# Optimization experiments

Measured on AMD Instinct MI355X. Metric: run time of the kernel, lower is better.

## Reference

```python
import jax, jax.numpy as jnp
import numpy as np

HIDDEN = 256
B, SQ, SKV = 8, 2048, 2048
SCALE = float(np.sqrt(HIDDEN / 2.0))  # module uses sqrt(hidden_dim/2)


def setup_inputs() -> dict:
    key = jax.random.key(0)
    ks = jax.random.split(key, 9)
    s = 1.0 / np.sqrt(HIDDEN)
    return {
        "query": jax.random.normal(ks[0], (B, SQ, HIDDEN), jnp.float32),
        "key": jax.random.normal(ks[1], (B, SKV, HIDDEN), jnp.float32),
        "value": jax.random.normal(ks[2], (B, SKV, HIDDEN), jnp.float32),
        "Wq": jax.random.uniform(ks[3], (HIDDEN, HIDDEN), jnp.float32, -s, s),
        "bq": jax.random.uniform(ks[4], (HIDDEN,), jnp.float32, -s, s),
        "Wk": jax.random.uniform(ks[5], (HIDDEN, HIDDEN), jnp.float32, -s, s),
        "bk": jax.random.uniform(ks[6], (HIDDEN,), jnp.float32, -s, s),
        "Wv": jax.random.uniform(ks[7], (HIDDEN, HIDDEN), jnp.float32, -s, s),
        "bv": jax.random.uniform(ks[8], (HIDDEN,), jnp.float32, -s, s),
    }


def reference(query, key, value, Wq, bq, Wk, bk, Wv, bv):
    # Linear projections (torch Linear: x @ W.T + b)
    Q = jnp.einsum('bsd,ed->bse', query, Wq) + bq  # [B,SQ,H]
    K = jnp.einsum('bsd,ed->bse', key, Wk) + bk    # [B,SKV,H]
    V = jnp.einsum('bsd,ed->bse', value, Wv) + bv  # [B,SKV,H]
    scores = jnp.einsum('bqd,bkd->bqk', Q, K) / SCALE  # [B,SQ,SKV]
    weights = jax.nn.softmax(scores, axis=-1)
    return jnp.einsum('bqk,bkd->bqd', weights, V)  # [B,SQ,H]
```

## Files before the change

### kernel.cpp

```cpp
#include <hip/hip_runtime.h>

#define HID 256
#define NB 8
#define SQL 2048
#define SKV 2048
#define SPLIT 4
#define KPB (SKV / SPLIT)
#define KVB 64
#define NT (KPB / KVB)
#define NROW (NB * SQL)

typedef __attribute__((ext_vector_type(8))) short bf16x8;
typedef __attribute__((ext_vector_type(4))) float f32x4;
typedef __attribute__((ext_vector_type(16))) float f32x16;

static __device__ __forceinline__ unsigned short f2bf(float x) {
  union { float f; unsigned int u; } v; v.f = x;
  unsigned int r = v.u + 0x7FFFu + ((v.u >> 16) & 1u);
  return (unsigned short)(r >> 16);
}

__global__ void wconv_kernel(const float* __restrict__ Wq, const float* __restrict__ Wk,
                             const float* __restrict__ Wv, unsigned short* __restrict__ out) {
  int i = blockIdx.x * blockDim.x + threadIdx.x;
  if (i >= 3 * HID * HID) return;
  const float* src = (i < HID * HID) ? Wq : (i < 2 * HID * HID ? Wk : Wv);
  out[i] = f2bf(src[i & (HID * HID - 1)]);
}

__global__ __launch_bounds__(512, 4) void proj_kernel(
    const float* __restrict__ query, const float* __restrict__ key, const float* __restrict__ value,
    const unsigned short* __restrict__ Wb,
    const float* __restrict__ bq, const float* __restrict__ bk, const float* __restrict__ bv,
    unsigned short* __restrict__ Qb, unsigned short* __restrict__ Kb, unsigned short* __restrict__ Vtb) {
  __shared__ __align__(16) char wl[65536];
  int tid = threadIdx.x;
  int wave = tid >> 6, lane = tid & 63, lr = lane & 15, lg = lane >> 4;
  int blk = blockIdx.x;
  int mat = blk >> 8;
  int rem = blk & 255;
  int b = rem >> 5;
  int rt = (rem >> 1) & 15;
  int et = rem & 1;

  const float* X = (mat == 0) ? query : (mat == 1 ? key : value);
  const float* bias = (mat == 0) ? bq : (mat == 1 ? bk : bv);
  const char* Wsrc = (const char*)(Wb + mat * HID * HID + et * 128 * HID);

#pragma unroll
  for (int i = 0; i < 8; i++) {
    int c = i * 512 + tid;
    int e = c >> 5;
    int glo = e * 512 + (((c & 31) ^ (e & 7)) << 4);
    __builtin_amdgcn_global_load_lds(
        (const __attribute__((address_space(1))) unsigned int*)(Wsrc + glo),
        (__attribute__((address_space(3))) unsigned int*)(wl + c * 16), 16, 0, 0);
  }

  int row_a = rt * 128 + wave * 16 + lr;
  const float* xrow = X + ((size_t)(b * SQL + row_a)) * HID;
  bf16x8 af[8];
#pragma unroll
  for (int s = 0; s < 8; s++) {
    const float4* p = (const float4*)(xrow + s * 32 + lg * 8);
    float4 x0 = p[0], x1 = p[1];
    bf16x8 a;
    a[0] = (short)f2bf(x0.x); a[1] = (short)f2bf(x0.y); a[2] = (short)f2bf(x0.z); a[3] = (short)f2bf(x0.w);
    a[4] = (short)f2bf(x1.x); a[5] = (short)f2bf(x1.y); a[6] = (short)f2bf(x1.z); a[7] = (short)f2bf(x1.w);
    af[s] = a;
  }
  __syncthreads();

  int row_c = rt * 128 + wave * 16 + lg * 4;
#pragma unroll
  for (int eo = 0; eo < 8; eo++) {
    f32x4 acc = (f32x4){0.f, 0.f, 0.f, 0.f};
    int eL = eo * 16 + lr;
#pragma unroll
    for (int sl = 0; sl < 8; sl++) {
      bf16x8 bfr = *(const bf16x8*)(wl + eL * 512 + (((sl * 4 + lg) ^ (eL & 7)) << 4));
      acc = __builtin_amdgcn_mfma_f32_16x16x32_bf16(af[sl], bfr, acc, 0, 0, 0);
    }
    int e = et * 128 + eo * 16 + lr;
    float bv_ = bias[e];
    if (mat < 2) {
      unsigned short* dst = (mat == 0 ? Qb : Kb) + (size_t)(b * SQL) * HID;
#pragma unroll
      for (int i = 0; i < 4; i++)
        dst[(size_t)(row_c + i) * HID + e] = f2bf(acc[i] + bv_);
    } else {
      ushort4 v;
      v.x = f2bf(acc[0] + bv_); v.y = f2bf(acc[1] + bv_);
      v.z = f2bf(acc[2] + bv_); v.w = f2bf(acc[3] + bv_);
      *(ushort4*)(Vtb + ((size_t)(b * HID + e)) * SKV + row_c) = v;
    }
  }
}

__global__ __launch_bounds__(512, 2) void attn_kernel(
    const unsigned short* __restrict__ Qb, const unsigned short* __restrict__ Kb,
    const unsigned short* __restrict__ Vtb, unsigned short* __restrict__ Op,
    float* __restrict__ Ml) {
  extern __shared__ char smem[];
  int tid = threadIdx.x;
  int wave = tid >> 6, lane = tid & 63, l31 = lane & 31, h = lane >> 5;
  int L = (blockIdx.x & 7) * 32 + (blockIdx.x >> 3);
  int b = L >> 5, sp = (L >> 3) & 3, qt = L & 7;
  int q0 = qt * 256 + wave * 32;

  const char* Kc0 = (const char*)Kb + ((size_t)b * SKV + (size_t)sp * KPB) * (HID * 2);
  const char* Vc0 = (const char*)Vtb + (size_t)b * HID * SKV * 2 + (size_t)sp * KPB * 2;

  auto stage = [&](int t, char* kb, char* vb) {
    const char* Ks = Kc0 + t * (KVB * HID * 2);
    const char* Vs = Vc0 + t * (KVB * 2);
#pragma unroll
    for (int i = 0; i < 4; i++) {
      int g = i * 512 + tid;
      int ky = g >> 5, cs = g & 31;
      __builtin_amdgcn_global_load_lds(
          (const __attribute__((address_space(1))) unsigned int*)(Ks + ky * 512 + ((cs ^ (ky & 31)) << 4)),
          (__attribute__((address_space(3))) unsigned int*)(kb + g * 16), 16, 0, 0);
    }
#pragma unroll
    for (int i = 0; i < 4; i++) {
      int g = i * 512 + tid;
      int d = g >> 3, cs = g & 7;
      __builtin_amdgcn_global_load_lds(
          (const __attribute__((address_space(1))) unsigned int*)(Vs + (size_t)d * (SKV * 2) + ((cs ^ (d & 7)) << 4)),
          (__attribute__((address_space(3))) unsigned int*)(vb + g * 16), 16, 0, 0);
    }
  };

  bf16x8 qf[16];
  {
    const unsigned short* qrow = Qb + ((size_t)(b * SQL + q0 + l31)) * HID + h * 8;
#pragma unroll
    for (int s = 0; s < 16; s++) qf[s] = *(const bf16x8*)(qrow + s * 16);
  }

  f32x16 acc[8];
#pragma unroll
  for (int dt = 0; dt < 8; dt++)
#pragma unroll
    for (int j = 0; j < 16; j++) acc[dt][j] = 0.f;

  float m = -1e30f, lsum = 0.f;
  const float kC = 1.44269504088896341f / 11.3137084989847604f;

  auto substep = [&](const char* kb, const char* vb, int kt) {
    f32x16 p;
#pragma unroll
    for (int j = 0; j < 16; j++) p[j] = 0.f;
#pragma unroll
    for (int s = 0; s < 16; s++) {
      bf16x8 kf = *(const bf16x8*)(kb + (kt * 32 + l31) * 512 + (((2 * s + h) ^ l31) << 4));
      p = __builtin_amdgcn_mfma_f32_32x32x16_bf16(kf, qf[s], p, 0, 0, 0);
    }

    float tmax = p[0];
#pragma unroll
    for (int j = 1; j < 16; j++) tmax = fmaxf(tmax, p[j]);
    tmax = fmaxf(tmax, __shfl_xor(tmax, 32, 64));
    float msc = tmax * kC;
    if (!__all(msc <= m + 8.0f)) {
      float mn = fmaxf(m, msc);
      float al = exp2f(m - mn);
      lsum *= al;
      m = mn;
#pragma unroll
      for (int r = 0; r < 16; r++) {
        int qp = (r & 3) + 8 * (r >> 2) + 4 * h;
        float ar = __shfl(al, qp, 64);
#pragma unroll
        for (int dt = 0; dt < 8; dt++) acc[dt][r] *= ar;
      }
    }
#pragma unroll
    for (int j = 0; j < 16; j++) p[j] = exp2f(fmaf(p[j], kC, -m));
    float ts = 0.f;
#pragma unroll
    for (int j = 0; j < 16; j++) ts += p[j];
    ts += __shfl_xor(ts, 32, 64);
    lsum += ts;

#pragma unroll
    for (int k2 = 0; k2 < 2; k2++) {
      unsigned P0, P1, P2, P3;
      asm("v_cvt_pk_bf16_f32 %0, %1, %2" : "=v"(P0) : "v"(p[k2 * 8 + 0]), "v"(p[k2 * 8 + 1]));
      asm("v_cvt_pk_bf16_f32 %0, %1, %2" : "=v"(P1) : "v"(p[k2 * 8 + 2]), "v"(p[k2 * 8 + 3]));
      asm("v_cvt_pk_bf16_f32 %0, %1, %2" : "=v"(P2) : "v"(p[k2 * 8 + 4]), "v"(p[k2 * 8 + 5]));
      asm("v_cvt_pk_bf16_f32 %0, %1, %2" : "=v"(P3) : "v"(p[k2 * 8 + 6]), "v"(p[k2 * 8 + 7]));
      asm("v_permlane32_swap_b32 %0, %1" : "+v"(P0), "+v"(P2));
      asm("v_permlane32_swap_b32 %0, %1" : "+v"(P1), "+v"(P3));
      union { unsigned u[4]; bf16x8 v; } pa;
      pa.u[0] = P0; pa.u[1] = P1; pa.u[2] = P2; pa.u[3] = P3;
      int c = kt * 4 + k2 * 2 + h;
#pragma unroll
      for (int dt = 0; dt < 8; dt++) {
        bf16x8 vf = *(const bf16x8*)(vb + (dt * 32 + l31) * 128 + (((c ^ (l31 & 7)) & 7) << 4));
        acc[dt] = __builtin_amdgcn_mfma_f32_32x32x16_bf16(pa.v, vf, acc[dt], 0, 0, 0);
      }
    }
  };

  stage(0, smem, smem + 65536);
  for (int t = 0; t < NT; t++) {
    const char* kb = smem + (t & 1) * 32768;
    const char* vb = smem + 65536 + (t & 1) * 32768;
    if (t + 1 < NT) {
      stage(t + 1, smem + ((t + 1) & 1) * 32768, smem + 65536 + ((t + 1) & 1) * 32768);
      asm volatile("s_waitcnt vmcnt(8)" ::: "memory");
    } else {
      asm volatile("s_waitcnt vmcnt(0)" ::: "memory");
    }
    __builtin_amdgcn_s_barrier();
    __builtin_amdgcn_sched_barrier(0);
    substep(kb, vb, 0);
    substep(kb, vb, 1);
    __builtin_amdgcn_s_barrier();
  }

  if (h == 0) {
    float2 ml; ml.x = m; ml.y = lsum;
    *(float2*)(Ml + ((size_t)sp * NROW + (size_t)b * SQL + q0 + l31) * 2) = ml;
  }
#pragma unroll
  for (int r = 0; r < 16; r++) {
    int qp = (r & 3) + 8 * (r >> 2) + 4 * h;
    float linv = 1.0f / __shfl(lsum, qp, 64);
    size_t row = (size_t)b * SQL + q0 + qp;
#pragma unroll
    for (int dt = 0; dt < 8; dt++) {
      union { _Float16 hf; unsigned short u; } cv;
      cv.hf = (_Float16)(acc[dt][r] * linv);
      Op[((size_t)sp * NROW + row) * HID + dt * 32 + l31] = cv.u;
    }
  }
}

__global__ __launch_bounds__(256) void comb_kernel(const unsigned short* __restrict__ Op,
                                                   const float* __restrict__ Ml,
                                                   float* __restrict__ out) {
  int idx = blockIdx.x * 256 + threadIdx.x;
  int row = idx >> 6;
  int d0 = (idx & 63) << 2;
  float mv[SPLIT], lv[SPLIT];
#pragma unroll
  for (int s = 0; s < SPLIT; s++) {
    float2 ml = *(const float2*)(Ml + ((size_t)s * NROW + row) * 2);
    mv[s] = ml.x; lv[s] = ml.y;
  }
  float M = mv[0];
#pragma unroll
  for (int s = 1; s < SPLIT; s++) M = fmaxf(M, mv[s]);
  float W = 0.f, w[SPLIT];
#pragma unroll
  for (int s = 0; s < SPLIT; s++) { w[s] = lv[s] * exp2f(mv[s] - M); W += w[s]; }
  float wi = 1.0f / W;
  float o0 = 0.f, o1 = 0.f, o2 = 0.f, o3 = 0.f;
#pragma unroll
  for (int s = 0; s < SPLIT; s++) {
    ushort4 u = *(const ushort4*)(Op + ((size_t)s * NROW + row) * HID + d0);
    union { unsigned short us; _Float16 hf; } c0, c1, c2, c3;
    c0.us = u.x; c1.us = u.y; c2.us = u.z; c3.us = u.w;
    o0 += w[s] * (float)c0.hf; o1 += w[s] * (float)c1.hf;
    o2 += w[s] * (float)c2.hf; o3 += w[s] * (float)c3.hf;
  }
  float4 res; res.x = o0 * wi; res.y = o1 * wi; res.z = o2 * wi; res.w = o3 * wi;
  *(float4*)(out + (size_t)row * HID + d0) = res;
}

extern "C" void kernel_launch(void* const* d_in, const int* in_sizes, int n_in,
                              void* d_out, int out_size, void* d_ws, size_t ws_size,
                              hipStream_t stream) {
  const float* query = (const float*)d_in[0];
  const float* key   = (const float*)d_in[1];
  const float* value = (const float*)d_in[2];
  const float* Wq = (const float*)d_in[3];
  const float* bq = (const float*)d_in[4];
  const float* Wk = (const float*)d_in[5];
  const float* bk = (const float*)d_in[6];
  const float* Wv = (const float*)d_in[7];
  const float* bv = (const float*)d_in[8];

  char* ws = (char*)d_ws;
  unsigned short* Wb  = (unsigned short*)ws;
  unsigned short* Qb  = (unsigned short*)(ws + 393216);
  unsigned short* Kb  = Qb + (size_t)NB * SQL * HID;
  unsigned short* Vtb = Kb + (size_t)NB * SKV * HID;
  unsigned short* Op  = Vtb + (size_t)NB * HID * SKV;
  float* Ml = (float*)(Op + (size_t)SPLIT * NROW * HID);

  hipLaunchKernelGGL(wconv_kernel, dim3(768), dim3(256), 0, stream, Wq, Wk, Wv, Wb);
  hipLaunchKernelGGL(proj_kernel, dim3(768), dim3(512), 0, stream,
                     query, key, value, Wb, bq, bk, bv, Qb, Kb, Vtb);
  hipLaunchKernelGGL(attn_kernel, dim3(256), dim3(512), 131072, stream, Qb, Kb, Vtb, Op, Ml);
  hipLaunchKernelGGL(comb_kernel, dim3(4096), dim3(256), 0, stream, Op, Ml, (float*)d_out);
}
```

Baseline: 103.1 us.

## Software-pipeline QK of the next tile with PV of the previous tile

Attention blocks shrink to 4 waves covering 128 query rows, and the KV tile shrinks to 32 keys. The main loop is reordered so the QK MFMAs for tile t are issued next to the PV MFMAs for tile t-1. K uses double buffering and V uses triple buffering, and each iteration needs a single barrier instead of two. Global-to-LDS staging offsets are precomputed per thread, and the V LDS swizzle is changed. The goal is to hide softmax latency and barrier stalls behind matrix work, at the cost of more live registers (the bf16 P fragments are carried across iterations) and twice as many loop iterations.

```diff
diff --git a/kernel.cpp b/kernel.cpp
--- a/kernel.cpp
+++ b/kernel.cpp
@@ -6,7 +6,7 @@
 #define SKV 2048
 #define SPLIT 4
 #define KPB (SKV / SPLIT)
-#define KVB 64
+#define KVB 32
 #define NT (KPB / KVB)
 #define NROW (NB * SQL)
 
@@ -97,39 +97,47 @@
   }
 }
 
-__global__ __launch_bounds__(512, 2) void attn_kernel(
+__global__ __launch_bounds__(256, 2) void attn_kernel(
     const unsigned short* __restrict__ Qb, const unsigned short* __restrict__ Kb,
     const unsigned short* __restrict__ Vtb, unsigned short* __restrict__ Op,
     float* __restrict__ Ml) {
   extern __shared__ char smem[];
   int tid = threadIdx.x;
   int wave = tid >> 6, lane = tid & 63, l31 = lane & 31, h = lane >> 5;
-  int L = (blockIdx.x & 7) * 32 + (blockIdx.x >> 3);
-  int b = L >> 5, sp = (L >> 3) & 3, qt = L & 7;
-  int q0 = qt * 256 + wave * 32;
-
-  const char* Kc0 = (const char*)Kb + ((size_t)b * SKV + (size_t)sp * KPB) * (HID * 2);
-  const char* Vc0 = (const char*)Vtb + (size_t)b * HID * SKV * 2 + (size_t)sp * KPB * 2;
+  int L = (blockIdx.x & 7) * 64 + (blockIdx.x >> 3);
+  int b = L >> 6, sp = (L >> 4) & 3, qt = L & 15;
+  int q0 = qt * 128 + wave * 32;
+
+  const char* Kc0 = (const char*)(Kb + ((size_t)b * SKV + (size_t)sp * KPB) * HID);
+  const char* Vc0 = (const char*)(Vtb + (size_t)b * HID * SKV + (size_t)sp * KPB);
+
+  int offK[4], offV[4];
+#pragma unroll
+  for (int i = 0; i < 4; i++) {
+    int idx = i * 256 + tid;
+    int ky = idx >> 5, cs = idx & 31;
+    offK[i] = ky * 512 + ((cs ^ ky) << 4);
+    int rv = idx >> 3, pp = idx & 7;
+    int p = pp ^ (rv & 7);
+    int d = 2 * rv + (p >> 2), c = p & 3;
+    offV[i] = d * (SKV * 2) + c * 16;
+  }
 
   auto stage = [&](int t, char* kb, char* vb) {
     const char* Ks = Kc0 + t * (KVB * HID * 2);
     const char* Vs = Vc0 + t * (KVB * 2);
 #pragma unroll
-    for (int i = 0; i < 4; i++) {
-      int g = i * 512 + tid;
-      int ky = g >> 5, cs = g & 31;
+    for (int i = 0; i < 4; i++)
       __builtin_amdgcn_global_load_lds(
-          (const __attribute__((address_space(1))) unsigned int*)(Ks + ky * 512 + ((cs ^ (ky & 31)) << 4)),
-          (__attribute__((address_space(3))) unsigned int*)(kb + g * 16), 16, 0, 0);
-    }
-#pragma unroll
-    for (int i = 0; i < 4; i++) {
-      int g = i * 512 + tid;
-      int d = g >> 3, cs = g & 7;
+          (const __attribute__((address_space(1))) unsigned int*)(Ks + offK[i]),
+          (__attribute__((address_space(3))) unsigned int*)(kb + (i * 256 + tid) * 16),
+          16, 0, 0);
+#pragma unroll
+    for (int i = 0; i < 4; i++)
       __builtin_amdgcn_global_load_lds(
-          (const __attribute__((address_space(1))) unsigned int*)(Vs + (size_t)d * (SKV * 2) + ((cs ^ (d & 7)) << 4)),
-          (__attribute__((address_space(3))) unsigned int*)(vb + g * 16), 16, 0, 0);
-    }
+          (const __attribute__((address_space(1))) unsigned int*)(Vs + offV[i]),
+          (__attribute__((address_space(3))) unsigned int*)(vb + (i * 256 + tid) * 16),
+          16, 0, 0);
   };
 
   bf16x8 qf[16];
@@ -147,17 +155,35 @@
 
   float m = -1e30f, lsum = 0.f;
   const float kC = 1.44269504088896341f / 11.3137084989847604f;
-
-  auto substep = [&](const char* kb, const char* vb, int kt) {
+  bf16x8 pa0, pa1;
+
+  auto qk = [&](const char* kb) {
     f32x16 p;
 #pragma unroll
     for (int j = 0; j < 16; j++) p[j] = 0.f;
 #pragma unroll
     for (int s = 0; s < 16; s++) {
-      bf16x8 kf = *(const bf16x8*)(kb + (kt * 32 + l31) * 512 + (((2 * s + h) ^ l31) << 4));
+      bf16x8 kf = *(const bf16x8*)(kb + l31 * 512 + (((2 * s + h) ^ l31) << 4));
       p = __builtin_amdgcn_mfma_f32_32x32x16_bf16(kf, qf[s], p, 0, 0, 0);
     }
-
+    return p;
+  };
+
+  auto pv = [&](const char* vb) {
+#pragma unroll
+    for (int k2 = 0; k2 < 2; k2++) {
+      bf16x8 pav = (k2 == 0) ? pa0 : pa1;
+#pragma unroll
+      for (int dt = 0; dt < 8; dt++) {
+        int d = dt * 32 + l31;
+        int slot = (((d & 1) * 4 + k2 * 2 + h) ^ ((d >> 1) & 7));
+        bf16x8 vf = *(const bf16x8*)(vb + (d >> 1) * 128 + (slot << 4));
+        acc[dt] = __builtin_amdgcn_mfma_f32_32x32x16_bf16(pav, vf, acc[dt], 0, 0, 0);
+      }
+    }
+  };
+
+  auto sm = [&](f32x16 p) {
     float tmax = p[0];
 #pragma unroll
     for (int j = 1; j < 16; j++) tmax = fmaxf(tmax, p[j]);
@@ -184,42 +210,48 @@
     ts += __shfl_xor(ts, 32, 64);
     lsum += ts;
 
-#pragma unroll
-    for (int k2 = 0; k2 < 2; k2++) {
-      unsigned P0, P1, P2, P3;
-      asm("v_cvt_pk_bf16_f32 %0, %1, %2" : "=v"(P0) : "v"(p[k2 * 8 + 0]), "v"(p[k2 * 8 + 1]));
-      asm("v_cvt_pk_bf16_f32 %0, %1, %2" : "=v"(P1) : "v"(p[k2 * 8 + 2]), "v"(p[k2 * 8 + 3]));
-      asm("v_cvt_pk_bf16_f32 %0, %1, %2" : "=v"(P2) : "v"(p[k2 * 8 + 4]), "v"(p[k2 * 8 + 5]));
-      asm("v_cvt_pk_bf16_f32 %0, %1, %2" : "=v"(P3) : "v"(p[k2 * 8 + 6]), "v"(p[k2 * 8 + 7]));
-      asm("v_permlane32_swap_b32 %0, %1" : "+v"(P0), "+v"(P2));
-      asm("v_permlane32_swap_b32 %0, %1" : "+v"(P1), "+v"(P3));
-      union { unsigned u[4]; bf16x8 v; } pa;
-      pa.u[0] = P0; pa.u[1] = P1; pa.u[2] = P2; pa.u[3] = P3;
-      int c = kt * 4 + k2 * 2 + h;
-#pragma unroll
-      for (int dt = 0; dt < 8; dt++) {
-        bf16x8 vf = *(const bf16x8*)(vb + (dt * 32 + l31) * 128 + (((c ^ (l31 & 7)) & 7) << 4));
-        acc[dt] = __builtin_amdgcn_mfma_f32_32x32x16_bf16(pa.v, vf, acc[dt], 0, 0, 0);
-      }
-    }
+    unsigned P0, P1, P2, P3, P4, P5, P6, P7;
+    asm("v_cvt_pk_bf16_f32 %0, %1, %2" : "=v"(P0) : "v"(p[0]), "v"(p[1]));
+    asm("v_cvt_pk_bf16_f32 %0, %1, %2" : "=v"(P1) : "v"(p[2]), "v"(p[3]));
+    asm("v_cvt_pk_bf16_f32 %0, %1, %2" : "=v"(P2) : "v"(p[4]), "v"(p[5]));
+    asm("v_cvt_pk_bf16_f32 %0, %1, %2" : "=v"(P3) : "v"(p[6]), "v"(p[7]));
+    asm("v_cvt_pk_bf16_f32 %0, %1, %2" : "=v"(P4) : "v"(p[8]), "v"(p[9]));
+    asm("v_cvt_pk_bf16_f32 %0, %1, %2" : "=v"(P5) : "v"(p[10]), "v"(p[11]));
+    asm("v_cvt_pk_bf16_f32 %0, %1, %2" : "=v"(P6) : "v"(p[12]), "v"(p[13]));
+    asm("v_cvt_pk_bf16_f32 %0, %1, %2" : "=v"(P7) : "v"(p[14]), "v"(p[15]));
+    asm("v_permlane32_swap_b32 %0, %1" : "+v"(P0), "+v"(P2));
+    asm("v_permlane32_swap_b32 %0, %1" : "+v"(P1), "+v"(P3));
+    asm("v_permlane32_swap_b32 %0, %1" : "+v"(P4), "+v"(P6));
+    asm("v_permlane32_swap_b32 %0, %1" : "+v"(P5), "+v"(P7));
+    union { unsigned u[4]; bf16x8 v; } a0, a1;
+    a0.u[0] = P0; a0.u[1] = P1; a0.u[2] = P2; a0.u[3] = P3;
+    a1.u[0] = P4; a1.u[1] = P5; a1.u[2] = P6; a1.u[3] = P7;
+    pa0 = a0.v; pa1 = a1.v;
   };
 
-  stage(0, smem, smem + 65536);
-  for (int t = 0; t < NT; t++) {
-    const char* kb = smem + (t & 1) * 32768;
-    const char* vb = smem + 65536 + (t & 1) * 32768;
-    if (t + 1 < NT) {
-      stage(t + 1, smem + ((t + 1) & 1) * 32768, smem + 65536 + ((t + 1) & 1) * 32768);
-      asm volatile("s_waitcnt vmcnt(8)" ::: "memory");
-    } else {
-      asm volatile("s_waitcnt vmcnt(0)" ::: "memory");
-    }
-    __builtin_amdgcn_s_barrier();
-    __builtin_amdgcn_sched_barrier(0);
-    substep(kb, vb, 0);
-    substep(kb, vb, 1);
-    __builtin_amdgcn_s_barrier();
-  }
+  stage(0, smem, smem + 32768);
+  __syncthreads();
+  stage(1, smem + 16384, smem + 32768 + 16384);
+  {
+    f32x16 p = qk(smem);
+    sm(p);
+  }
+  __syncthreads();
+
+  int vprev = 0, vnext = 2;
+  for (int t = 1; t < NT; t++) {
+    const char* kb = smem + ((t & 1) << 14);
+    const char* vbp = smem + 32768 + (vprev << 14);
+    if (t + 1 < NT)
+      stage(t + 1, smem + (((t + 1) & 1) << 14), smem + 32768 + (vnext << 14));
+    f32x16 p = qk(kb);
+    pv(vbp);
+    sm(p);
+    vprev = (vprev == 2) ? 0 : vprev + 1;
+    vnext = (vnext == 2) ? 0 : vnext + 1;
+    __syncthreads();
+  }
+  pv(smem + 32768 + (vprev << 14));
 
   if (h == 0) {
     float2 ml; ml.x = m; ml.y = lsum;
@@ -295,6 +327,6 @@
   hipLaunchKernelGGL(wconv_kernel, dim3(768), dim3(256), 0, stream, Wq, Wk, Wv, Wb);
   hipLaunchKernelGGL(proj_kernel, dim3(768), dim3(512), 0, stream,
                      query, key, value, Wb, bq, bk, bv, Qb, Kb, Vtb);
-  hipLaunchKernelGGL(attn_kernel, dim3(256), dim3(512), 131072, stream, Qb, Kb, Vtb, Op, Ml);
+  hipLaunchKernelGGL(attn_kernel, dim3(512), dim3(256), 81920, stream, Qb, Kb, Vtb, Op, Ml);
   hipLaunchKernelGGL(comb_kernel, dim3(4096), dim3(256), 0, stream, Op, Ml, (float*)d_out);
 }
```

Result: faster. 100.0 us (-2.9%).
